# Kernel optimization log

Hardware: AMD Instinct MI355X
Metric: run time of the kernel (lower is better)

## Reference

```python
import jax, jax.numpy as jnp
import numpy as np

NUM_HEADS = 4
NUM_GROUPS = 8
EPS = 1e-5


def setup_inputs() -> dict:
    key = jax.random.key(0)
    ks = jax.random.split(key, 5)
    B, C, H, W = 16, 512, 32, 32
    s = 1.0 / np.sqrt(C)
    return {
        "x": jax.random.normal(ks[0], (B, C, H, W), dtype=jnp.float32),
        "norm_w": jnp.ones((C,), jnp.float32),
        "norm_b": jnp.zeros((C,), jnp.float32),
        "q_w": jax.random.normal(ks[1], (C, C), jnp.float32) * s,
        "q_b": jnp.zeros((C,), jnp.float32),
        "k_w": jax.random.normal(ks[2], (C, C), jnp.float32) * s,
        "k_b": jnp.zeros((C,), jnp.float32),
        "v_w": jax.random.normal(ks[3], (C, C), jnp.float32) * s,
        "v_b": jnp.zeros((C,), jnp.float32),
        "p_w": jax.random.normal(ks[4], (C, C), jnp.float32) * s,
        "p_b": jnp.zeros((C,), jnp.float32),
    }


def _group_norm(x, w, b):
    # x: (B, C, N) -> GroupNorm over (C//G, N) per group
    B, C, N = x.shape
    g = x.reshape(B, NUM_GROUPS, C // NUM_GROUPS, N)
    mean = g.mean(axis=(2, 3), keepdims=True)
    var = g.var(axis=(2, 3), keepdims=True)
    g = (g - mean) * jax.lax.rsqrt(var + EPS)
    x = g.reshape(B, C, N)
    return x * w[None, :, None] + b[None, :, None]


def reference(x, norm_w, norm_b, q_w, q_b, k_w, k_b, v_w, v_b, p_w, p_b):
    B, C, H, W = x.shape
    N = H * W
    Ch = C // NUM_HEADS  # channels per head
    h = _group_norm(x.reshape(B, C, N), norm_w, norm_b)
    # 1x1 Conv1d == channel matmul: (o c, b c n -> b o n)
    q = jnp.einsum('oc,bcn->bon', q_w, h) + q_b[None, :, None]
    k = jnp.einsum('oc,bcn->bon', k_w, h) + k_b[None, :, None]
    v = jnp.einsum('oc,bcn->bon', v_w, h) + v_b[None, :, None]
    q = q.reshape(B, NUM_HEADS, Ch, N)
    k = k.reshape(B, NUM_HEADS, Ch, N)
    v = v.reshape(B, NUM_HEADS, Ch, N)
    attn = jnp.einsum('bhcn,bhcm->bhnm', q, k) * (1.0 / np.sqrt(Ch))
    attn = jax.nn.softmax(attn, axis=-1)
    out = jnp.einsum('bhnm,bhcm->bhcn', attn, v).reshape(B, C, N)
    out = jnp.einsum('oc,bcn->bon', p_w, out) + p_b[None, :, None]
    return x + out.reshape(B, C, H, W)
```

## Files before the change

kernel.cpp:

```cpp
#include <hip/hip_runtime.h>
#include <hip/hip_bf16.h>
#include <math.h>

#define B_    16
#define C_    512
#define N_    1024
#define G_    8
#define HEADS 4
#define CH    128
#define EPS   1e-5f

typedef __attribute__((ext_vector_type(8))) short short8;
typedef __attribute__((ext_vector_type(4))) float f32x4;
typedef __attribute__((ext_vector_type(16))) float f32x16;
typedef __attribute__((ext_vector_type(4))) int i32x4;

__device__ __forceinline__ unsigned short f2bf(float f) {
  union { float f; unsigned int i; } x; x.f = f;
  unsigned int r = x.i + 0x7FFFu + ((x.i >> 16) & 1u);
  return (unsigned short)(r >> 16);
}

__global__ __launch_bounds__(256) void gn_part_conv(const float* __restrict__ x,
                                                    float2* __restrict__ psum,
                                                    const float* __restrict__ qw, const float* __restrict__ kw,
                                                    const float* __restrict__ vw, const float* __restrict__ pw,
                                                    const float* __restrict__ qb, const float* __restrict__ kb,
                                                    unsigned short* __restrict__ wbf,
                                                    float* __restrict__ qkb) {
  int blk = blockIdx.x;
  if (blk < 512) {
    const float4* p4 = (const float4*)(x + (size_t)blk * 16384);
    float s = 0.f, ss = 0.f;
    for (int i = threadIdx.x; i < 4096; i += 256) {
      float4 v = p4[i];
      s  += v.x + v.y + v.z + v.w;
      ss += v.x * v.x + v.y * v.y + v.z * v.z + v.w * v.w;
    }
    for (int o = 32; o; o >>= 1) { s += __shfl_down(s, o); ss += __shfl_down(ss, o); }
    __shared__ float ls[4], lss[4];
    int wid = threadIdx.x >> 6, lane = threadIdx.x & 63;
    if (lane == 0) { ls[wid] = s; lss[wid] = ss; }
    __syncthreads();
    if (threadIdx.x == 0) {
      float2 r;
      r.x = (ls[0] + ls[1]) + (ls[2] + ls[3]);
      r.y = (lss[0] + lss[1]) + (lss[2] + lss[3]);
      psum[blk] = r;
    }
  } else {
    const int n = C_ * C_;
    int i = (blk - 512) * 256 + threadIdx.x;
    wbf[i]         = f2bf(qw[i]);
    wbf[n + i]     = f2bf(kw[i]);
    wbf[2 * n + i] = f2bf(vw[i]);
    wbf[3 * n + i] = f2bf(pw[i]);
    if (i < 1024) qkb[i] = (i < 512) ? qb[i] : kb[i - 512];
  }
}

__global__ __launch_bounds__(256) void gn_apply(const float* __restrict__ x,
                                                const float2* __restrict__ psum,
                                                const float* __restrict__ gw,
                                                const float* __restrict__ gb,
                                                unsigned short* __restrict__ hT) {
  __shared__ float T[64][65];
  int b = blockIdx.z, c0 = blockIdx.y * 64, n0 = blockIdx.x * 64;
  int bg = b * G_ + (c0 >> 6);
  float2 p0 = psum[bg * 4 + 0], p1 = psum[bg * 4 + 1];
  float2 p2 = psum[bg * 4 + 2], p3 = psum[bg * 4 + 3];
  const float inv = 1.f / ((C_ / G_) * N_);
  float mean = ((p0.x + p1.x) + (p2.x + p3.x)) * inv;
  float var  = ((p0.y + p1.y) + (p2.y + p3.y)) * inv - mean * mean;
  float rstd = rsqrtf(var + EPS);
  int t = threadIdx.x;
  for (int it = 0; it < 4; it++) {
    int L = it * 256 + t;
    int cc = L >> 4, nf = L & 15;
    float4 v = *(const float4*)&x[((size_t)b * C_ + c0 + cc) * N_ + n0 + nf * 4];
    float sw = gw[c0 + cc] * rstd, sb = gb[c0 + cc] - mean * sw;
    T[cc][nf * 4 + 0] = v.x * sw + sb;
    T[cc][nf * 4 + 1] = v.y * sw + sb;
    T[cc][nf * 4 + 2] = v.z * sw + sb;
    T[cc][nf * 4 + 3] = v.w * sw + sb;
  }
  __syncthreads();
  for (int it = 0; it < 4; it++) {
    int L = it * 256 + t;
    int nn = L >> 4, cv = L & 15;
    ushort4 o;
    o.x = f2bf(T[cv * 4 + 0][nn]);
    o.y = f2bf(T[cv * 4 + 1][nn]);
    o.z = f2bf(T[cv * 4 + 2][nn]);
    o.w = f2bf(T[cv * 4 + 3][nn]);
    *(ushort4*)&hT[((size_t)b * N_ + n0 + nn) * C_ + c0 + cv * 4] = o;
  }
}

__global__ __launch_bounds__(256) void gemm_qkv(const unsigned short* __restrict__ hT,
                                                const unsigned short* __restrict__ wbf,
                                                const float* __restrict__ qkb,
                                                const float* __restrict__ vb,
                                                unsigned short* __restrict__ qkT,
                                                unsigned short* __restrict__ vv) {
  __shared__ __align__(16) unsigned short As[128 * 64];
  __shared__ __align__(16) unsigned short Bs[128 * 64];
  const int lin0 = blockIdx.x;
  const bool isV = lin0 >= 1024;
  const int lin = isV ? lin0 - 1024 : lin0;
  const int b = (lin & 7) * 2 + ((lin >> 3) & 1);
  const int rest = lin >> 4;
  const int bx = rest & 7, by = rest >> 3;
  const int i0 = by * 128, j0 = bx * 128;
  const long NC = (long)N_ * C_;
  const int n_w = C_ * C_;
  const unsigned short* Ab;
  const unsigned short* Bb;
  const float* bias;
  unsigned short* out;
  long oBS;
  if (isV) {
    Ab = wbf + 2 * n_w + (size_t)i0 * C_;
    Bb = hT + (size_t)b * NC + (size_t)j0 * C_;
    bias = vb; out = vv; oBS = NC;
  } else {
    Ab = hT + (size_t)b * NC + (size_t)i0 * C_;
    Bb = wbf + (size_t)j0 * C_;
    bias = qkb; out = qkT; oBS = (long)N_ * 1024;
  }
  const int t = threadIdx.x, w = t >> 6, l = t & 63;
  const int wi = (w >> 1) * 64, wj = (w & 1) * 64;
  const int lr = l & 15, lk = (l >> 4) * 8;
  const int srow = l >> 3, scol = (l & 7) * 8;

  f32x4 acc[4][4];
  const f32x4 zf = {0.f, 0.f, 0.f, 0.f};
#pragma unroll
  for (int m = 0; m < 4; m++)
#pragma unroll
    for (int n = 0; n < 4; n++) acc[m][n] = zf;

  for (int kt = 0; kt < C_; kt += 64) {
    __syncthreads();
#pragma unroll
    for (int i = 0; i < 4; i++) {
      int seg = w * 4 + i;
      int row = seg * 8 + srow;
      __builtin_amdgcn_global_load_lds(
          (const __attribute__((address_space(1))) void*)&Ab[(size_t)row * C_ + kt + scol],
          (__attribute__((address_space(3))) void*)&As[seg * 512], 16, 0, 0);
      __builtin_amdgcn_global_load_lds(
          (const __attribute__((address_space(1))) void*)&Bb[(size_t)row * C_ + kt + scol],
          (__attribute__((address_space(3))) void*)&Bs[seg * 512], 16, 0, 0);
    }
    __syncthreads();
#pragma unroll
    for (int ks = 0; ks < 64; ks += 32) {
      short8 af[4], bf[4];
#pragma unroll
      for (int m = 0; m < 4; m++) af[m] = *(const short8*)&As[(wi + m * 16 + lr) * 64 + ks + lk];
#pragma unroll
      for (int n = 0; n < 4; n++) bf[n] = *(const short8*)&Bs[(wj + n * 16 + lr) * 64 + ks + lk];
#pragma unroll
      for (int m = 0; m < 4; m++)
#pragma unroll
        for (int n = 0; n < 4; n++)
          acc[m][n] = __builtin_amdgcn_mfma_f32_16x16x32_bf16(af[m], bf[n], acc[m][n], 0, 0, 0);
    }
  }

  int rbase = (l >> 4) * 4;
#pragma unroll
  for (int m = 0; m < 4; m++) {
    int ig = i0 + wi + m * 16 + rbase;
#pragma unroll
    for (int n = 0; n < 4; n++) {
      int jg = j0 + wj + n * 16 + lr;
#pragma unroll
      for (int r = 0; r < 4; r++) {
        float vvv = acc[m][n][r];
        vvv += isV ? bias[ig + r] : bias[jg];
        size_t oidx = (size_t)b * oBS + (size_t)(ig + r) * 1024 + jg;
        out[oidx] = f2bf(vvv);
      }
    }
  }
}

__global__ __launch_bounds__(256) void gemm_p(const unsigned short* __restrict__ A,
                                              const unsigned short* __restrict__ Bt,
                                              const float* __restrict__ bias,
                                              const float* __restrict__ resid,
                                              float* __restrict__ out) {
  __shared__ __align__(16) unsigned short As[128 * 64];
  __shared__ __align__(16) unsigned short Bs[128 * 64];
  const int lin = blockIdx.x;
  const int b = (lin & 7) * 2 + ((lin >> 3) & 1);
  const int rest = lin >> 4;
  const int bx = rest & 7, by = rest >> 3;
  const int i0 = by * 128, j0 = bx * 128;
  const long NC = (long)N_ * C_;
  const unsigned short* Ab = A + (size_t)i0 * C_;
  const unsigned short* Bb = Bt + (size_t)b * NC + (size_t)j0 * C_;
  const int t = threadIdx.x, w = t >> 6, l = t & 63;
  const int wi = (w >> 1) * 64, wj = (w & 1) * 64;
  const int lr = l & 15, lk = (l >> 4) * 8;
  const int srow = l >> 3, scol = (l & 7) * 8;

  f32x4 acc[4][4];
  const f32x4 zf = {0.f, 0.f, 0.f, 0.f};
#pragma unroll
  for (int m = 0; m < 4; m++)
#pragma unroll
    for (int n = 0; n < 4; n++) acc[m][n] = zf;

  for (int kt = 0; kt < C_; kt += 64) {
    __syncthreads();
#pragma unroll
    for (int i = 0; i < 4; i++) {
      int seg = w * 4 + i;
      int row = seg * 8 + srow;
      __builtin_amdgcn_global_load_lds(
          (const __attribute__((address_space(1))) void*)&Ab[(size_t)row * C_ + kt + scol],
          (__attribute__((address_space(3))) void*)&As[seg * 512], 16, 0, 0);
      __builtin_amdgcn_global_load_lds(
          (const __attribute__((address_space(1))) void*)&Bb[(size_t)row * C_ + kt + scol],
          (__attribute__((address_space(3))) void*)&Bs[seg * 512], 16, 0, 0);
    }
    __syncthreads();
#pragma unroll
    for (int ks = 0; ks < 64; ks += 32) {
      short8 af[4], bf[4];
#pragma unroll
      for (int m = 0; m < 4; m++) af[m] = *(const short8*)&As[(wi + m * 16 + lr) * 64 + ks + lk];
#pragma unroll
      for (int n = 0; n < 4; n++) bf[n] = *(const short8*)&Bs[(wj + n * 16 + lr) * 64 + ks + lk];
#pragma unroll
      for (int m = 0; m < 4; m++)
#pragma unroll
        for (int n = 0; n < 4; n++)
          acc[m][n] = __builtin_amdgcn_mfma_f32_16x16x32_bf16(af[m], bf[n], acc[m][n], 0, 0, 0);
    }
  }

  int rbase = (l >> 4) * 4;
#pragma unroll
  for (int m = 0; m < 4; m++) {
    int ig = i0 + wi + m * 16 + rbase;
#pragma unroll
    for (int n = 0; n < 4; n++) {
      int jg = j0 + wj + n * 16 + lr;
#pragma unroll
      for (int r = 0; r < 4; r++) {
        float vv = acc[m][n][r] + bias[ig + r];
        size_t oidx = (size_t)b * NC + (size_t)(ig + r) * N_ + jg;
        out[oidx] = vv + resid[oidx];
      }
    }
  }
}

__global__ __launch_bounds__(256, 2) void attn_kernel(const unsigned short* __restrict__ qkT,
                                                      const unsigned short* __restrict__ v,
                                                      unsigned short* __restrict__ aoT) {
  __shared__ __align__(16) unsigned short Ks[2][64 * 128];
  __shared__ __align__(16) unsigned short Vs[3][128 * 64];
  const int t = threadIdx.x, w = t >> 6, l = t & 63;
  const int h = l >> 5, l31 = l & 31, l7 = l & 7;
  const int lin = blockIdx.x;
  const int bh = (lin & 7) * 8 + ((lin >> 3) & 7);
  const int qt = lin >> 6;
  const int b = bh >> 2, hd = bh & 3, c0h = hd * CH;
  const int qg = qt * 128 + w * 32 + l31;
  const float sc2 = 0.08838834764831845f * 1.4426950408889634f;
  const float THRRAW = 11.5f / sc2;

  short8 qf[8];
  const unsigned short* qrow = qkT + ((size_t)b * N_ + qg) * 1024 + c0h;
#pragma unroll
  for (int kc = 0; kc < 8; kc++) qf[kc] = *(const short8*)&qrow[kc * 16 + h * 8];

  f32x16 o[4];
#pragma unroll
  for (int ct = 0; ct < 4; ct++) o[ct] = (f32x16)(0.f);
  float m = -INFINITY, lsum = 0.f;

  const unsigned short* ksrcp[4];
  const unsigned short* vsrcp[4];
#pragma unroll
  for (int i = 0; i < 4; i++) {
    int seg = w * 4 + i;
    int rowK = seg * 4 + (l >> 4);
    int gcK = (l & 15) ^ (rowK & 7);
    ksrcp[i] = qkT + ((size_t)b * N_ + rowK) * 1024 + 512 + c0h + gcK * 8;
    int rowV = seg * 8 + (l >> 3);
    int gcV = (l & 7) ^ (rowV & 7);
    vsrcp[i] = v + ((size_t)b * C_ + c0h + rowV) * N_ + gcV * 8;
  }
  auto stage = [&](int kbuf, int vbuf) {
#pragma unroll
    for (int i = 0; i < 4; i++) {
      int seg = w * 4 + i;
      __builtin_amdgcn_global_load_lds((const __attribute__((address_space(1))) void*)ksrcp[i],
                                       (__attribute__((address_space(3))) void*)&Ks[kbuf][seg * 512],
                                       16, 0, 0);
      ksrcp[i] += (size_t)64 * 1024;
      __builtin_amdgcn_global_load_lds((const __attribute__((address_space(1))) void*)vsrcp[i],
                                       (__attribute__((address_space(3))) void*)&Vs[vbuf][seg * 512],
                                       16, 0, 0);
      vsrcp[i] += 64;
    }
  };

  stage(0, 0);
  stage(1, 1);
  __syncthreads();

  f32x16 st0 = (f32x16)(0.f), st1 = (f32x16)(0.f);
  {
    const unsigned short* KsB = &Ks[0][0];
#pragma unroll
    for (int kc = 0; kc < 8; kc++) {
      short8 kf0 = *(const short8*)&KsB[l31 * 128 + (((2 * kc + h) ^ l7) * 8)];
      short8 kf1 = *(const short8*)&KsB[(32 + l31) * 128 + (((2 * kc + h) ^ l7) * 8)];
      st0 = __builtin_amdgcn_mfma_f32_32x32x16_bf16(kf0, qf[kc], st0, 0, 0, 0);
      st1 = __builtin_amdgcn_mfma_f32_32x32x16_bf16(kf1, qf[kc], st1, 0, 0, 0);
    }
  }
  __syncthreads();

  for (int tt = 0; tt < 16; tt++) {
    if (tt < 14) stage(tt & 1, (tt + 2) % 3);

    float tr[16];
#pragma unroll
    for (int r = 0; r < 16; r++) tr[r] = fmaxf(st0[r], st1[r]);
#pragma unroll
    for (int s = 8; s >= 1; s >>= 1)
#pragma unroll
      for (int r = 0; r < s; r++) tr[r] = fmaxf(tr[r], tr[r + s]);
    float pmax = fmaxf(tr[0], __shfl_xor(tr[0], 32));

    bool skip = __all(pmax <= m + THRRAW);
    float mnew = skip ? m : fmaxf(m, pmax);
    float alpha = skip ? 1.f : exp2f((m - mnew) * sc2);
    float mb = mnew * sc2;
    m = mnew;

    float psg[4];
    short8 pf[4];
#pragma unroll
    for (int g = 0; g < 4; g++) {
      const int e0 = (g & 1) * 8;
      float p0, p1, p2, p3, p4, p5, p6, p7;
      if (g < 2) {
        p0 = exp2f(fmaf(st0[e0 + 0], sc2, -mb)); p1 = exp2f(fmaf(st0[e0 + 1], sc2, -mb));
        p2 = exp2f(fmaf(st0[e0 + 2], sc2, -mb)); p3 = exp2f(fmaf(st0[e0 + 3], sc2, -mb));
        p4 = exp2f(fmaf(st0[e0 + 4], sc2, -mb)); p5 = exp2f(fmaf(st0[e0 + 5], sc2, -mb));
        p6 = exp2f(fmaf(st0[e0 + 6], sc2, -mb)); p7 = exp2f(fmaf(st0[e0 + 7], sc2, -mb));
      } else {
        p0 = exp2f(fmaf(st1[e0 + 0], sc2, -mb)); p1 = exp2f(fmaf(st1[e0 + 1], sc2, -mb));
        p2 = exp2f(fmaf(st1[e0 + 2], sc2, -mb)); p3 = exp2f(fmaf(st1[e0 + 3], sc2, -mb));
        p4 = exp2f(fmaf(st1[e0 + 4], sc2, -mb)); p5 = exp2f(fmaf(st1[e0 + 5], sc2, -mb));
        p6 = exp2f(fmaf(st1[e0 + 6], sc2, -mb)); p7 = exp2f(fmaf(st1[e0 + 7], sc2, -mb));
      }
      psg[g] = ((p0 + p1) + (p2 + p3)) + ((p4 + p5) + (p6 + p7));
      unsigned int x, x2, y, y2;
      asm("v_cvt_pk_bf16_f32 %0, %1, %2" : "=v"(x)  : "v"(p0), "v"(p1));
      asm("v_cvt_pk_bf16_f32 %0, %1, %2" : "=v"(x2) : "v"(p2), "v"(p3));
      asm("v_cvt_pk_bf16_f32 %0, %1, %2" : "=v"(y)  : "v"(p4), "v"(p5));
      asm("v_cvt_pk_bf16_f32 %0, %1, %2" : "=v"(y2) : "v"(p6), "v"(p7));
      asm("v_permlane32_swap_b32 %0, %1" : "+v"(x), "+v"(y));
      asm("v_permlane32_swap_b32 %0, %1" : "+v"(x2), "+v"(y2));
      i32x4 pwv = {(int)x, (int)x2, (int)y, (int)y2};
      pf[g] = __builtin_bit_cast(short8, pwv);
    }
    float ps = (psg[0] + psg[1]) + (psg[2] + psg[3]);
    ps += __shfl_xor(ps, 32);
    lsum = lsum * alpha + ps;

    if (!skip) {
#pragma unroll
      for (int ct = 0; ct < 4; ct++)
#pragma unroll
        for (int r = 0; r < 16; r++) o[ct][r] *= alpha;
    }

    const unsigned short* VsB = &Vs[tt % 3][0];
    __builtin_amdgcn_s_setprio(1);
    if (tt < 15) {
      const unsigned short* KsN = &Ks[(tt + 1) & 1][0];
      f32x16 nst0 = (f32x16)(0.f), nst1 = (f32x16)(0.f);
#pragma unroll
      for (int kc = 0; kc < 8; kc++) {
        short8 kf0 = *(const short8*)&KsN[l31 * 128 + (((2 * kc + h) ^ l7) * 8)];
        short8 kf1 = *(const short8*)&KsN[(32 + l31) * 128 + (((2 * kc + h) ^ l7) * 8)];
        nst0 = __builtin_amdgcn_mfma_f32_32x32x16_bf16(kf0, qf[kc], nst0, 0, 0, 0);
        nst1 = __builtin_amdgcn_mfma_f32_32x32x16_bf16(kf1, qf[kc], nst1, 0, 0, 0);
        {
          int p = 2 * kc;
          int ct = p & 3, g = p >> 2;
          short8 vf = *(const short8*)&VsB[(ct * 32 + l31) * 64 + (((2 * g + h) ^ l7) * 8)];
          o[ct] = __builtin_amdgcn_mfma_f32_32x32x16_bf16(vf, pf[g], o[ct], 0, 0, 0);
          p = 2 * kc + 1;
          ct = p & 3; g = p >> 2;
          vf = *(const short8*)&VsB[(ct * 32 + l31) * 64 + (((2 * g + h) ^ l7) * 8)];
          o[ct] = __builtin_amdgcn_mfma_f32_32x32x16_bf16(vf, pf[g], o[ct], 0, 0, 0);
        }
      }
      __builtin_amdgcn_s_setprio(0);
      __syncthreads();
      st0 = nst0; st1 = nst1;
    } else {
#pragma unroll
      for (int p = 0; p < 16; p++) {
        int ct = p & 3, g = p >> 2;
        short8 vf = *(const short8*)&VsB[(ct * 32 + l31) * 64 + (((2 * g + h) ^ l7) * 8)];
        o[ct] = __builtin_amdgcn_mfma_f32_32x32x16_bf16(vf, pf[g], o[ct], 0, 0, 0);
      }
      __builtin_amdgcn_s_setprio(0);
    }
  }

  float rn = 1.f / lsum;
  unsigned short* orow = aoT + ((size_t)b * N_ + qg) * C_ + c0h;
#pragma unroll
  for (int ct = 0; ct < 4; ct++)
#pragma unroll
    for (int u = 0; u < 4; u++) {
      ushort4 ov;
      ov.x = f2bf(o[ct][u * 4 + 0] * rn);
      ov.y = f2bf(o[ct][u * 4 + 1] * rn);
      ov.z = f2bf(o[ct][u * 4 + 2] * rn);
      ov.w = f2bf(o[ct][u * 4 + 3] * rn);
      *(ushort4*)&orow[ct * 32 + u * 8 + h * 4] = ov;
    }
}

extern "C" void kernel_launch(void* const* d_in, const int* in_sizes, int n_in,
                              void* d_out, int out_size, void* d_ws, size_t ws_size,
                              hipStream_t stream) {
  const float* x  = (const float*)d_in[0];
  const float* nw = (const float*)d_in[1];
  const float* nb = (const float*)d_in[2];
  const float* qw = (const float*)d_in[3];
  const float* qb = (const float*)d_in[4];
  const float* kw = (const float*)d_in[5];
  const float* kb = (const float*)d_in[6];
  const float* vw = (const float*)d_in[7];
  const float* vb = (const float*)d_in[8];
  const float* pw = (const float*)d_in[9];
  const float* pb = (const float*)d_in[10];

  char* ws = (char*)d_ws;
  unsigned short* wbf  = (unsigned short*)ws;
  float2*         psum = (float2*)(ws + 0x200000);
  float*          qkb  = (float*)(ws + 0x201000);
  unsigned short* hT   = (unsigned short*)(ws + 0x202000);
  unsigned short* qkT  = (unsigned short*)(ws + 0x1202000);
  unsigned short* vv   = (unsigned short*)(ws + 0x3202000);
  unsigned short* aoT  = hT;

  const int n_w = C_ * C_;

  gn_part_conv<<<dim3(1536), 256, 0, stream>>>(x, psum, qw, kw, vw, pw, qb, kb, wbf, qkb);
  gn_apply<<<dim3(N_ / 64, C_ / 64, B_), 256, 0, stream>>>(x, psum, nw, nb, hT);

  gemm_qkv<<<dim3(1536), 256, 0, stream>>>(hT, wbf, qkb, vb, qkT, vv);

  attn_kernel<<<dim3(512), 256, 0, stream>>>(qkT, vv, aoT);

  gemm_p<<<dim3(512), 256, 0, stream>>>(wbf + 3 * n_w, aoT, pb, x, (float*)d_out);
}
```

Measured before the change: 137.7 us.

## Double-buffer LDS tiles in QKV and projection GEMMs to overlap loads with MFMA

Both bf16 GEMM kernels now keep two LDS buffers per operand. The next K-tile is prefetched with global_load_lds while MFMAs run on the current tile, and each iteration needs one barrier instead of two. Source pointers are precomputed and advanced by 64 elements per stage, which removes per-iteration address math. The cost is twice the LDS per block (64KB), which can lower the number of resident blocks per CU. The overlap also depends on the compiler not inserting conservative vmcnt waits before the LDS reads.

```diff
diff --git a/kernel.cpp b/kernel.cpp
--- a/kernel.cpp
+++ b/kernel.cpp
@@ -103,8 +103,8 @@
                                                 const float* __restrict__ vb,
                                                 unsigned short* __restrict__ qkT,
                                                 unsigned short* __restrict__ vv) {
-  __shared__ __align__(16) unsigned short As[128 * 64];
-  __shared__ __align__(16) unsigned short Bs[128 * 64];
+  __shared__ __align__(16) unsigned short As[2][128 * 64];
+  __shared__ __align__(16) unsigned short Bs[2][128 * 64];
   const int lin0 = blockIdx.x;
   const bool isV = lin0 >= 1024;
   const int lin = isV ? lin0 - 1024 : lin0;
@@ -133,6 +133,30 @@
   const int lr = l & 15, lk = (l >> 4) * 8;
   const int srow = l >> 3, scol = (l & 7) * 8;
 
+  const unsigned short* asrc[4];
+  const unsigned short* bsrc[4];
+#pragma unroll
+  for (int i = 0; i < 4; i++) {
+    int seg = w * 4 + i;
+    int row = seg * 8 + srow;
+    asrc[i] = &Ab[(size_t)row * C_ + scol];
+    bsrc[i] = &Bb[(size_t)row * C_ + scol];
+  }
+  auto stage = [&](int buf) {
+#pragma unroll
+    for (int i = 0; i < 4; i++) {
+      int seg = w * 4 + i;
+      __builtin_amdgcn_global_load_lds((const __attribute__((address_space(1))) void*)asrc[i],
+                                       (__attribute__((address_space(3))) void*)&As[buf][seg * 512],
+                                       16, 0, 0);
+      asrc[i] += 64;
+      __builtin_amdgcn_global_load_lds((const __attribute__((address_space(1))) void*)bsrc[i],
+                                       (__attribute__((address_space(3))) void*)&Bs[buf][seg * 512],
+                                       16, 0, 0);
+      bsrc[i] += 64;
+    }
+  };
+
   f32x4 acc[4][4];
   const f32x4 zf = {0.f, 0.f, 0.f, 0.f};
 #pragma unroll
@@ -140,27 +164,19 @@
 #pragma unroll
     for (int n = 0; n < 4; n++) acc[m][n] = zf;
 
-  for (int kt = 0; kt < C_; kt += 64) {
+  stage(0);
+  for (int kt8 = 0; kt8 < 8; kt8++) {
     __syncthreads();
-#pragma unroll
-    for (int i = 0; i < 4; i++) {
-      int seg = w * 4 + i;
-      int row = seg * 8 + srow;
-      __builtin_amdgcn_global_load_lds(
-          (const __attribute__((address_space(1))) void*)&Ab[(size_t)row * C_ + kt + scol],
-          (__attribute__((address_space(3))) void*)&As[seg * 512], 16, 0, 0);
-      __builtin_amdgcn_global_load_lds(
-          (const __attribute__((address_space(1))) void*)&Bb[(size_t)row * C_ + kt + scol],
-          (__attribute__((address_space(3))) void*)&Bs[seg * 512], 16, 0, 0);
-    }
-    __syncthreads();
+    if (kt8 < 7) stage((kt8 + 1) & 1);
+    const unsigned short* AsB = &As[kt8 & 1][0];
+    const unsigned short* BsB = &Bs[kt8 & 1][0];
 #pragma unroll
     for (int ks = 0; ks < 64; ks += 32) {
       short8 af[4], bf[4];
 #pragma unroll
-      for (int m = 0; m < 4; m++) af[m] = *(const short8*)&As[(wi + m * 16 + lr) * 64 + ks + lk];
-#pragma unroll
-      for (int n = 0; n < 4; n++) bf[n] = *(const short8*)&Bs[(wj + n * 16 + lr) * 64 + ks + lk];
+      for (int m = 0; m < 4; m++) af[m] = *(const short8*)&AsB[(wi + m * 16 + lr) * 64 + ks + lk];
+#pragma unroll
+      for (int n = 0; n < 4; n++) bf[n] = *(const short8*)&BsB[(wj + n * 16 + lr) * 64 + ks + lk];
 #pragma unroll
       for (int m = 0; m < 4; m++)
 #pragma unroll
@@ -192,8 +208,8 @@
                                               const float* __restrict__ bias,
                                               const float* __restrict__ resid,
                                               float* __restrict__ out) {
-  __shared__ __align__(16) unsigned short As[128 * 64];
-  __shared__ __align__(16) unsigned short Bs[128 * 64];
+  __shared__ __align__(16) unsigned short As[2][128 * 64];
+  __shared__ __align__(16) unsigned short Bs[2][128 * 64];
   const int lin = blockIdx.x;
   const int b = (lin & 7) * 2 + ((lin >> 3) & 1);
   const int rest = lin >> 4;
@@ -207,6 +223,30 @@
   const int lr = l & 15, lk = (l >> 4) * 8;
   const int srow = l >> 3, scol = (l & 7) * 8;
 
+  const unsigned short* asrc[4];
+  const unsigned short* bsrc[4];
+#pragma unroll
+  for (int i = 0; i < 4; i++) {
+    int seg = w * 4 + i;
+    int row = seg * 8 + srow;
+    asrc[i] = &Ab[(size_t)row * C_ + scol];
+    bsrc[i] = &Bb[(size_t)row * C_ + scol];
+  }
+  auto stage = [&](int buf) {
+#pragma unroll
+    for (int i = 0; i < 4; i++) {
+      int seg = w * 4 + i;
+      __builtin_amdgcn_global_load_lds((const __attribute__((address_space(1))) void*)asrc[i],
+                                       (__attribute__((address_space(3))) void*)&As[buf][seg * 512],
+                                       16, 0, 0);
+      asrc[i] += 64;
+      __builtin_amdgcn_global_load_lds((const __attribute__((address_space(1))) void*)bsrc[i],
+                                       (__attribute__((address_space(3))) void*)&Bs[buf][seg * 512],
+                                       16, 0, 0);
+      bsrc[i] += 64;
+    }
+  };
+
   f32x4 acc[4][4];
   const f32x4 zf = {0.f, 0.f, 0.f, 0.f};
 #pragma unroll
@@ -214,27 +254,19 @@
 #pragma unroll
     for (int n = 0; n < 4; n++) acc[m][n] = zf;
 
-  for (int kt = 0; kt < C_; kt += 64) {
+  stage(0);
+  for (int kt8 = 0; kt8 < 8; kt8++) {
     __syncthreads();
-#pragma unroll
-    for (int i = 0; i < 4; i++) {
-      int seg = w * 4 + i;
-      int row = seg * 8 + srow;
-      __builtin_amdgcn_global_load_lds(
-          (const __attribute__((address_space(1))) void*)&Ab[(size_t)row * C_ + kt + scol],
-          (__attribute__((address_space(3))) void*)&As[seg * 512], 16, 0, 0);
-      __builtin_amdgcn_global_load_lds(
-          (const __attribute__((address_space(1))) void*)&Bb[(size_t)row * C_ + kt + scol],
-          (__attribute__((address_space(3))) void*)&Bs[seg * 512], 16, 0, 0);
-    }
-    __syncthreads();
+    if (kt8 < 7) stage((kt8 + 1) & 1);
+    const unsigned short* AsB = &As[kt8 & 1][0];
+    const unsigned short* BsB = &Bs[kt8 & 1][0];
 #pragma unroll
     for (int ks = 0; ks < 64; ks += 32) {
       short8 af[4], bf[4];
 #pragma unroll
-      for (int m = 0; m < 4; m++) af[m] = *(const short8*)&As[(wi + m * 16 + lr) * 64 + ks + lk];
-#pragma unroll
-      for (int n = 0; n < 4; n++) bf[n] = *(const short8*)&Bs[(wj + n * 16 + lr) * 64 + ks + lk];
+      for (int m = 0; m < 4; m++) af[m] = *(const short8*)&AsB[(wi + m * 16 + lr) * 64 + ks + lk];
+#pragma unroll
+      for (int n = 0; n < 4; n++) bf[n] = *(const short8*)&BsB[(wj + n * 16 + lr) * 64 + ks + lk];
 #pragma unroll
       for (int m = 0; m < 4; m++)
 #pragma unroll
```

New measurement: 156.2 us. +13.5%, slower.
